# Kernel optimization log

Measured on AMD Instinct MI355X. Metric: run time of the kernel, lower is better.

## Reference

```python
import jax, jax.numpy as jnp
import numpy as np

B, T, D = 2, 2048, 1024
H = 16
HD = D // H  # 64


def _rope_tables(t_len, hd, dtype=jnp.float32):
    inv_freq = 1.0 / (10000.0 ** (jnp.arange(0, hd, 2, dtype=jnp.float32) / hd))
    freqs = jnp.outer(jnp.arange(t_len, dtype=jnp.float32), inv_freq)  # [T, hd/2]
    emb = jnp.concatenate([freqs, freqs], axis=-1)  # [T, hd]
    return emb.astype(dtype)


def _rotate_half(x):
    x1, x2 = jnp.split(x, 2, axis=-1)
    return jnp.concatenate([-x2, x1], axis=-1)


def setup_inputs() -> dict:
    key = jax.random.key(0)
    k1, k2, k3 = jax.random.split(key, 3)
    x = jax.random.normal(k1, (B, T, D), dtype=jnp.float32)
    w_qkv = jax.random.normal(k2, (D, 3 * D), dtype=jnp.float32) * (D ** -0.5)
    w_out = jax.random.normal(k3, (D, D), dtype=jnp.float32) * (D ** -0.5)
    return {"x": x, "w_qkv": w_qkv, "w_out": w_out}


def reference(x, w_qkv, w_out):
    Bc, Tc, Dc = x.shape
    scale = HD ** -0.5
    qkv = x @ w_qkv  # [B,T,3D]
    q, k, v = jnp.split(qkv, 3, axis=-1)
    # -> [B,H,T,hd]
    q = q.reshape(Bc, Tc, H, HD).transpose(0, 2, 1, 3)
    k = k.reshape(Bc, Tc, H, HD).transpose(0, 2, 1, 3)
    v = v.reshape(Bc, Tc, H, HD).transpose(0, 2, 1, 3)
    emb = _rope_tables(Tc, HD, x.dtype)  # [T,hd]
    cos = jnp.cos(emb)[None, None, :, :]
    sin = jnp.sin(emb)[None, None, :, :]
    q = q * cos + _rotate_half(q) * sin
    k = k * cos + _rotate_half(k) * sin
    attn = jnp.einsum('bhqd,bhkd->bhqk', q, k) * scale  # [B,H,T,T]
    causal = jnp.tril(jnp.ones((Tc, Tc), dtype=bool))
    attn = jnp.where(causal[None, None], attn, -jnp.inf)
    attn = jax.nn.softmax(attn, axis=-1)
    out = jnp.einsum('bhqk,bhkd->bhqd', attn, v)
    out = out.transpose(0, 2, 1, 3).reshape(Bc, Tc, Dc)
    return out @ w_out
```

## Files before the change

### kernel.cpp

```cpp
#include <hip/hip_runtime.h>

#define TSEQ 2048
#define DMODEL 1024
#define NHEAD 16
#define HDIM 64
#define NB 2
#define MROWS 4096
#define NQKV 3072
#define QSCALE 0.1803368801111204f
#define ROPE_C (13.2877123795494f / 32.0f)
#define NEGINF -3.0e38f

using s16x8 = __attribute__((ext_vector_type(8))) short;
using s16x4 = __attribute__((ext_vector_type(4))) short;
using f32x4 = __attribute__((ext_vector_type(4))) float;
using u32x2 = __attribute__((ext_vector_type(2))) unsigned int;

static __device__ __forceinline__ float b2f(unsigned short u) {
  union { unsigned int i; float f; } x; x.i = ((unsigned int)u) << 16; return x.f;
}
static __device__ __forceinline__ unsigned short f2b(float f) {
  unsigned int u = __float_as_uint(f);
  u += 0x7fffu + ((u >> 16) & 1u);
  return (unsigned short)(u >> 16);
}

#if __has_builtin(__builtin_amdgcn_exp2f)
#define EXP2(x) __builtin_amdgcn_exp2f(x)
#else
#define EXP2(x) exp2f(x)
#endif

typedef const __attribute__((address_space(1))) char gchar;
typedef __attribute__((address_space(3))) char lchar;
static __device__ __forceinline__ void gload_lds16(const void* g, void* l) {
  __builtin_amdgcn_global_load_lds((gchar*)g, (lchar*)l, 16, 0, 0);
}

__global__ __launch_bounds__(256) void k_prep(const float* __restrict__ x,
                                              short* __restrict__ xb,
                                              const float* __restrict__ wq,
                                              short* __restrict__ wqT,
                                              const float* __restrict__ wo,
                                              short* __restrict__ woT) {
  __shared__ float tile[32][33];
  const int blk = blockIdx.x;
  const int tid = threadIdx.x;
  if (blk < 4096) {
    const int i = blk * 256 + tid;
    const float4 v = ((const float4*)x)[i];
    s16x4 o;
    o.x = (short)f2b(v.x); o.y = (short)f2b(v.y);
    o.z = (short)f2b(v.z); o.w = (short)f2b(v.w);
    ((s16x4*)xb)[i] = o;
    return;
  }
  const float* in; short* out; int C, bx, by;
  if (blk < 7168) {
    const int l = blk - 4096; in = wq; out = wqT; C = NQKV;
    bx = l % 96; by = l / 96;
  } else {
    const int l = blk - 7168; in = wo; out = woT; C = DMODEL;
    bx = l & 31; by = l >> 5;
  }
  const int tx = tid & 31, ty4 = (tid >> 5) * 4;
#pragma unroll
  for (int i = 0; i < 4; ++i)
    tile[ty4 + i][tx] = in[(by * 32 + ty4 + i) * C + bx * 32 + tx];
  __syncthreads();
#pragma unroll
  for (int i = 0; i < 4; ++i)
    out[(bx * 32 + ty4 + i) * DMODEL + by * 32 + tx] = (short)f2b(tile[tx][ty4 + i]);
}

__global__ __launch_bounds__(256) void k_gemm_qkv(const short* __restrict__ A,
                                                  const short* __restrict__ BT,
                                                  short* __restrict__ Qo,
                                                  short* __restrict__ Ko,
                                                  short* __restrict__ Vt) {
  __shared__ __attribute__((aligned(16))) short As[128 * 64];
  __shared__ __attribute__((aligned(16))) short Bs[128 * 64];
  const int K = DMODEL;
  const int tid = threadIdx.x;
  const int wave = tid >> 6, lane = tid & 63, quad = lane >> 4, l15 = lane & 15;
  const int wm = (wave >> 1) * 64, wn = (wave & 1) * 64;
  const int bid = blockIdx.y * 24 + blockIdx.x;
  const int swz = (bid & 7) * 96 + (bid >> 3);
  const int bx = swz % 24, by = swz / 24;
  const int m0 = by * 128, n0 = bx * 128;
  f32x4 acc[4][4] = {};
  const char* Ab = (const char*)A;
  const char* Bb = (const char*)BT;
  char* AsB = (char*)As;
  char* BsB = (char*)Bs;
  int srow[4], scg[4], ssw[4];
#pragma unroll
  for (int p = 0; p < 4; ++p) {
    const int i = p * 256 + tid;
    srow[p] = i >> 3;
    scg[p] = i & 7;
    ssw[p] = scg[p] ^ (srow[p] & 7);
  }
#define QLOAD(k0v)                                                            \
  do {                                                                        \
    _Pragma("unroll")                                                         \
    for (int p = 0; p < 4; ++p) {                                             \
      ra[p] = *(const f32x4*)(Ab + ((long)(m0 + srow[p]) * K + (k0v)) * 2 + scg[p] * 16); \
      rb[p] = *(const f32x4*)(Bb + ((long)(n0 + srow[p]) * K + (k0v)) * 2 + scg[p] * 16); \
    }                                                                         \
  } while (0)
#define QWRITE()                                                              \
  do {                                                                        \
    _Pragma("unroll")                                                         \
    for (int p = 0; p < 4; ++p) {                                             \
      *(f32x4*)(AsB + srow[p] * 128 + ssw[p] * 16) = ra[p];                   \
      *(f32x4*)(BsB + srow[p] * 128 + ssw[p] * 16) = rb[p];                   \
    }                                                                         \
  } while (0)

  f32x4 ra[4], rb[4];
  const int nK = K / 64;
  QLOAD(0);
  QWRITE();
  __syncthreads();
  for (int kt = 0; kt < nK; ++kt) {
    if (kt + 1 < nK) QLOAD((kt + 1) * 64);
#pragma unroll
    for (int hf = 0; hf < 2; ++hf) {
      s16x8 af[4], bf[4];
#pragma unroll
      for (int i = 0; i < 4; ++i) {
        const int rowa = wm + i * 16 + l15;
        af[i] = *(const s16x8*)(AsB + rowa * 128 + (((hf * 4 + quad) ^ (rowa & 7)) * 16));
        const int rowb = wn + i * 16 + l15;
        bf[i] = *(const s16x8*)(BsB + rowb * 128 + (((hf * 4 + quad) ^ (rowb & 7)) * 16));
      }
#pragma unroll
      for (int i = 0; i < 4; ++i)
#pragma unroll
        for (int j = 0; j < 4; ++j)
          acc[i][j] = __builtin_amdgcn_mfma_f32_16x16x32_bf16(af[i], bf[j], acc[i][j], 0, 0, 0);
    }
    asm volatile("s_waitcnt lgkmcnt(0)" ::: "memory");
    __builtin_amdgcn_s_barrier();
    if (kt + 1 < nK) {
      QWRITE();
      asm volatile("s_waitcnt lgkmcnt(0)" ::: "memory");
      __builtin_amdgcn_s_barrier();
    }
  }
#undef QLOAD
#undef QWRITE
  const int colbase = n0 + wn;
  const int region = colbase >> 10;
  const int hh = (colbase & 1023) >> 6;
  const int bq = m0 >> 11;
  const int tbase = (m0 & 2047) + wm;
  char* sw = (wave < 2) ? (AsB + wave * 8192) : (BsB + (wave - 2) * 8192);
  if (region == 2) {
#pragma unroll
    for (int i = 0; i < 4; ++i)
#pragma unroll
      for (int j = 0; j < 4; ++j) {
        const int d = j * 16 + l15;
        const int t0 = i * 16 + quad * 4;
        s16x4 w;
        w.x = (short)f2b(acc[i][j][0]);
        w.y = (short)f2b(acc[i][j][1]);
        w.z = (short)f2b(acc[i][j][2]);
        w.w = (short)f2b(acc[i][j][3]);
        *(s16x4*)(sw + d * 128 + ((((t0 >> 3) ^ (d & 7))) * 16) + (t0 & 7) * 2) = w;
      }
    short* dstv = Vt + (((long)(bq * NHEAD + hh) * HDIM) << 11);
#pragma unroll
    for (int p = 0; p < 8; ++p) {
      const int linear = p * 64 + lane;
      const int d = linear >> 3, c = linear & 7;
      const s16x8 v = *(const s16x8*)(sw + d * 128 + ((c ^ (d & 7)) * 16));
      *(s16x8*)(dstv + (((long)d) << 11) + tbase + c * 8) = v;
    }
  } else {
    if (region == 1) {
#pragma unroll
      for (int i = 0; i < 4; ++i)
#pragma unroll
        for (int j = 0; j < 2; ++j) {
          const int d = j * 16 + l15;
          const float inv = exp2f(-(float)d * ROPE_C);
#pragma unroll
          for (int r = 0; r < 4; ++r) {
            const int t = tbase + i * 16 + quad * 4 + r;
            float sn, cs;
            __sincosf((float)t * inv, &sn, &cs);
            const float a = acc[i][j][r];
            const float bv = acc[i][j + 2][r];
            acc[i][j][r]     = a * cs - bv * sn;
            acc[i][j + 2][r] = bv * cs + a * sn;
          }
        }
    }
#pragma unroll
    for (int i = 0; i < 4; ++i)
#pragma unroll
      for (int j = 0; j < 4; ++j)
#pragma unroll
        for (int r = 0; r < 4; ++r) {
          const int row = i * 16 + quad * 4 + r;
          const int col = j * 16 + l15;
          *(short*)(sw + row * 128 + ((((col >> 3) ^ (row & 7))) * 16) + (col & 7) * 2)
              = (short)f2b(acc[i][j][r]);
        }
    short* dst = (region ? Ko : Qo) + ((long)(bq * NHEAD + hh) * TSEQ + tbase) * HDIM;
#pragma unroll
    for (int p = 0; p < 8; ++p) {
      const int linear = p * 64 + lane;
      const int r = linear >> 3, c = linear & 7;
      const s16x8 v = *(const s16x8*)(sw + r * 128 + ((c ^ (r & 7)) * 16));
      *(s16x8*)(dst + (long)r * HDIM + c * 8) = v;
    }
  }
}

template <int IM, bool OUT_BF16>
__global__ __launch_bounds__(256) void k_gemm(const short* __restrict__ A,
                                              const short* __restrict__ BT,
                                              void* __restrict__ Cv,
                                              int M, int N, int K) {
  static_assert(IM == 2, "vmcnt literal assumes IM==2 (6 loads/thread)");
  __shared__ __attribute__((aligned(16))) short As[2][IM * 32 * 64];
  __shared__ __attribute__((aligned(16))) short Bs[2][128 * 64];
  const int tid = threadIdx.x;
  const int wave = tid >> 6, lane = tid & 63, quad = lane >> 4, l15 = lane & 15;
  const int wm = (wave >> 1) * (IM * 16), wn = (wave & 1) * 64;
  const int nwg = gridDim.x * gridDim.y;
  const int bid = blockIdx.y * gridDim.x + blockIdx.x;
  const int swz = (bid & 7) * (nwg >> 3) + (bid >> 3);
  const int bx = swz % gridDim.x, by = swz / gridDim.x;
  const int m0 = by * (IM * 32), n0 = bx * 128;
  f32x4 acc[IM][4] = {};
  const char* Ab = (const char*)A;
  const char* Bb = (const char*)BT;
  char* AsB = (char*)As;
  char* BsB = (char*)Bs;
  int srow[4], sg[4];
#pragma unroll
  for (int p = 0; p < 4; ++p) {
    const int i = p * 256 + tid;
    srow[p] = i >> 3;
    sg[p] = (i & 7) ^ (srow[p] & 7);
  }
#define GSTAGE(k0v, buf)                                                       \
  do {                                                                         \
    _Pragma("unroll")                                                          \
    for (int p = 0; p < IM; ++p) {                                             \
      const long go = ((long)(m0 + srow[p]) * K + (k0v)) * 2 + sg[p] * 16;     \
      gload_lds16(Ab + go, AsB + (buf) * (IM * 4096) + p * 4096 + wave * 1024);\
    }                                                                          \
    _Pragma("unroll")                                                          \
    for (int p = 0; p < 4; ++p) {                                              \
      const long go = ((long)(n0 + srow[p]) * K + (k0v)) * 2 + sg[p] * 16;     \
      gload_lds16(Bb + go, BsB + (buf) * 16384 + p * 4096 + wave * 1024);      \
    }                                                                          \
  } while (0)

  const int nK = K / 64;
  GSTAGE(0, 0);
  for (int kt = 0; kt < nK; ++kt) {
    const int cur = kt & 1;
    if (kt + 1 < nK) {
      GSTAGE((kt + 1) * 64, cur ^ 1);
      asm volatile("s_waitcnt vmcnt(6)" ::: "memory");
    } else {
      asm volatile("s_waitcnt vmcnt(0)" ::: "memory");
    }
    __builtin_amdgcn_s_barrier();
    const char* Ac = AsB + cur * (IM * 4096);
    const char* Bc = BsB + cur * 16384;
#pragma unroll
    for (int hf = 0; hf < 2; ++hf) {
      s16x8 af[IM], bf[4];
#pragma unroll
      for (int i = 0; i < IM; ++i) {
        const int rowa = wm + i * 16 + l15;
        af[i] = *(const s16x8*)(Ac + rowa * 128 + (((hf * 4 + quad) ^ (rowa & 7)) * 16));
      }
#pragma unroll
      for (int j = 0; j < 4; ++j) {
        const int rowb = wn + j * 16 + l15;
        bf[j] = *(const s16x8*)(Bc + rowb * 128 + (((hf * 4 + quad) ^ (rowb & 7)) * 16));
      }
#pragma unroll
      for (int i = 0; i < IM; ++i)
#pragma unroll
        for (int j = 0; j < 4; ++j)
          acc[i][j] = __builtin_amdgcn_mfma_f32_16x16x32_bf16(af[i], bf[j], acc[i][j], 0, 0, 0);
    }
    asm volatile("s_waitcnt lgkmcnt(0)" ::: "memory");
    __builtin_amdgcn_s_barrier();
  }
#undef GSTAGE
  if (OUT_BF16) {
#pragma unroll
    for (int i = 0; i < IM; ++i) {
      const int row = m0 + wm + i * 16 + quad * 4;
#pragma unroll
      for (int j = 0; j < 4; ++j) {
        const int col = n0 + wn + j * 16 + l15;
#pragma unroll
        for (int r = 0; r < 4; ++r)
          ((short*)Cv)[(long)(row + r) * N + col] = (short)f2b(acc[i][j][r]);
      }
    }
  } else {
    char* sw = (char*)Bs + wave * 8192;
#pragma unroll
    for (int i = 0; i < IM; ++i)
#pragma unroll
      for (int j = 0; j < 4; ++j)
#pragma unroll
        for (int r = 0; r < 4; ++r) {
          const int row = i * 16 + quad * 4 + r;
          const int col = j * 16 + l15;
          *(float*)(sw + row * 256 + ((((col >> 2) ^ (row & 7))) * 16) + (col & 3) * 4)
              = acc[i][j][r];
        }
    float* C = (float*)Cv;
#pragma unroll
    for (int p = 0; p < 8; ++p) {
      const int linear = p * 64 + lane;
      const int r = linear >> 4, c = linear & 15;
      const f32x4 v = *(const f32x4*)(sw + r * 256 + ((c ^ (r & 7)) * 16));
      *(f32x4*)(C + (long)(m0 + wm + r) * N + n0 + wn + c * 4) = v;
    }
  }
}

__global__ __launch_bounds__(512) __attribute__((amdgpu_waves_per_eu(4)))
void k_attn(const short* __restrict__ Qg,
            const short* __restrict__ Kg,
            const short* __restrict__ Vg,
            short* __restrict__ O) {
  __shared__ __attribute__((aligned(16))) short Ks[2][64 * 64];
  __shared__ __attribute__((aligned(16))) short Vs[2][64 * 64];
  __shared__ __attribute__((aligned(16))) short pl[8][16 * 64];
  const int bx = blockIdx.x, by = blockIdx.y;
  const int qi = ((by >> 4) & 1) ? (15 - bx) : bx;
  const int bh = by;
  const int b = bh >> 4, h = bh & 15;
  const int tid = threadIdx.x, wave = tid >> 6, lane = tid & 63;
  const int quad = lane >> 4, l15 = lane & 15;
  const char* Kb = (const char*)(Kg + (long)bh * TSEQ * HDIM);
  const char* Vb = (const char*)(Vg + (long)bh * HDIM * TSEQ);
  const short* Qb = Qg + (long)bh * TSEQ * HDIM;
  const int qr0 = qi * 128 + wave * 16;
  const s16x8 rq0 = *(const s16x8*)&Qb[(qr0 + l15) * HDIM + quad * 8];
  const s16x8 rq1 = *(const s16x8*)&Qb[(qr0 + l15) * HDIM + 32 + quad * 8];
  s16x8 aq0, aq1;
  {
    const float tf = (float)(qr0 + l15);
#pragma unroll
    for (int j = 0; j < 8; ++j) {
      const float inv = exp2f(-(float)(quad * 8 + j) * ROPE_C);
      float sn, cs;
      __sincosf(tf * inv, &sn, &cs);
      sn *= QSCALE; cs *= QSCALE;
      const float q0 = b2f((unsigned short)rq0[j]);
      const float q1 = b2f((unsigned short)rq1[j]);
      aq0[j] = (short)f2b(q0 * cs - q1 * sn);
      aq1[j] = (short)f2b(q1 * cs + q0 * sn);
    }
  }
  s16x8 ones;
#pragma unroll
  for (int j = 0; j < 8; ++j) ones[j] = (short)0x3F80;
  f32x4 o[4] = {};
  f32x4 zs = {};
  const int kr0 = tid >> 3, kg0 = (tid & 7) ^ (kr0 & 7);
  char* KsB = (char*)Ks;
  char* VsB = (char*)Vs;
  char* plwB = (char*)pl + wave * 2048;
  const int ldsw = wave * 1024;

#define STAGE(kjv, buf)                                                     \
  do {                                                                      \
    gload_lds16(Kb + (kjv) * 8192 + (kr0 * 8 + kg0) * 16,                   \
                KsB + (buf) * 8192 + ldsw);                                 \
    gload_lds16(Vb + (kjv) * 128 + kr0 * (TSEQ * 2) + kg0 * 16,             \
                VsB + (buf) * 8192 + ldsw);                                 \
  } while (0)

  STAGE(0, 0);

  const int kjmax = 2 * qi + 1;
  const int kjd = qr0 >> 6;
  for (int kj = 0; kj <= kjmax; ++kj) {
    const int cur = kj & 1;
    if (kj < kjmax) {
      STAGE(kj + 1, cur ^ 1);
      asm volatile("s_waitcnt vmcnt(2)" ::: "memory");
    } else {
      asm volatile("s_waitcnt vmcnt(0)" ::: "memory");
    }
    __builtin_amdgcn_s_barrier();
    if (kj <= kjd) {
      const char* kb = KsB + cur * 8192;
      const char* vb = VsB + cur * 8192;
      f32x4 s[4];
      __builtin_amdgcn_s_setprio(1);
#pragma unroll
      for (int j2 = 0; j2 < 4; ++j2) {
        const int row = j2 * 16 + l15;
        const s16x8 k0 = *(const s16x8*)(kb + row * 128 + ((quad ^ (row & 7)) * 16));
        const s16x8 k1 = *(const s16x8*)(kb + row * 128 + (((4 + quad) ^ (row & 7)) * 16));
        f32x4 z = {};
        z = __builtin_amdgcn_mfma_f32_16x16x32_bf16(k0, aq0, z, 0, 0, 0);
        z = __builtin_amdgcn_mfma_f32_16x16x32_bf16(k1, aq1, z, 0, 0, 0);
        s[j2] = z;
      }
      __builtin_amdgcn_s_setprio(0);
      if (kj == kjd) {
        const int qloc = (qr0 & 63) + l15;
#pragma unroll
        for (int j2 = 0; j2 < 4; ++j2)
#pragma unroll
          for (int r = 0; r < 4; ++r)
            if (j2 * 16 + quad * 4 + r > qloc) s[j2][r] = NEGINF;
      }
#pragma unroll
      for (int j2 = 0; j2 < 4; ++j2) {
        const unsigned int u0 = __float_as_uint(EXP2(s[j2][0])) & 0xffff0000u;
        const unsigned int u1 = __float_as_uint(EXP2(s[j2][1])) & 0xffff0000u;
        const unsigned int u2 = __float_as_uint(EXP2(s[j2][2])) & 0xffff0000u;
        const unsigned int u3 = __float_as_uint(EXP2(s[j2][3])) & 0xffff0000u;
        u32x2 w;
        w.x = (u0 >> 16) | u1;
        w.y = (u2 >> 16) | u3;
        const int t0 = j2 * 16 + quad * 4;
        *(u32x2*)(plwB + l15 * 128 + (((t0 >> 3) ^ (l15 & 7)) * 16) + (quad & 1) * 8) = w;
      }
      const s16x8 bp0 = *(const s16x8*)(plwB + l15 * 128 + ((quad ^ (l15 & 7)) * 16));
      const s16x8 bp1 = *(const s16x8*)(plwB + l15 * 128 + (((4 + quad) ^ (l15 & 7)) * 16));
      __builtin_amdgcn_s_setprio(1);
      zs = __builtin_amdgcn_mfma_f32_16x16x32_bf16(ones, bp0, zs, 0, 0, 0);
      zs = __builtin_amdgcn_mfma_f32_16x16x32_bf16(ones, bp1, zs, 0, 0, 0);
#pragma unroll
      for (int hs = 0; hs < 4; ++hs) {
        const int d = hs * 16 + l15;
        const s16x8 av0 = *(const s16x8*)(vb + d * 128 + ((quad ^ (d & 7)) * 16));
        const s16x8 av1 = *(const s16x8*)(vb + d * 128 + (((4 + quad) ^ (d & 7)) * 16));
        o[hs] = __builtin_amdgcn_mfma_f32_16x16x32_bf16(av0, bp0, o[hs], 0, 0, 0);
        o[hs] = __builtin_amdgcn_mfma_f32_16x16x32_bf16(av1, bp1, o[hs], 0, 0, 0);
      }
      __builtin_amdgcn_s_setprio(0);
    }
    asm volatile("s_waitcnt lgkmcnt(0)" ::: "memory");
    __builtin_amdgcn_s_barrier();
  }
#undef STAGE
  const float rinv = 1.0f / zs[0];
  const int t = qr0 + l15;
  short* Orow = O + (long)(b * TSEQ + t) * DMODEL + h * HDIM + quad * 4;
#pragma unroll
  for (int hs = 0; hs < 4; ++hs) {
    s16x4 w;
    w.x = (short)f2b(o[hs][0] * rinv);
    w.y = (short)f2b(o[hs][1] * rinv);
    w.z = (short)f2b(o[hs][2] * rinv);
    w.w = (short)f2b(o[hs][3] * rinv);
    *(s16x4*)(Orow + hs * 16) = w;
  }
}

extern "C" void kernel_launch(void* const* d_in, const int* in_sizes, int n_in,
                              void* d_out, int out_size, void* d_ws, size_t ws_size,
                              hipStream_t stream) {
  const float* x = (const float*)d_in[0];
  const float* w_qkv = (const float*)d_in[1];
  const float* w_out = (const float*)d_in[2];
  float* out = (float*)d_out;
  char* ws = (char*)d_ws;

  short* xb    = (short*)(ws);
  short* wqkvT = (short*)(ws + (8ll << 20));
  short* woutT = (short*)(ws + (14ll << 20));
  short* Qb    = (short*)(ws + (16ll << 20));
  short* Kb    = (short*)(ws + (24ll << 20));
  short* Vt    = (short*)(ws + (32ll << 20));
  short* Ob    = (short*)(ws + (40ll << 20));

  k_prep<<<dim3(8192), dim3(256), 0, stream>>>(x, xb, w_qkv, wqkvT, w_out, woutT);
  k_gemm_qkv<<<dim3(NQKV / 128, MROWS / 128), dim3(256), 0, stream>>>(
      xb, wqkvT, Qb, Kb, Vt);
  k_attn<<<dim3(TSEQ / 128, NB * NHEAD), dim3(512), 0, stream>>>(Qb, Kb, Vt, Ob);
  k_gemm<2, false><<<dim3(DMODEL / 128, MROWS / 64), dim3(256), 0, stream>>>(
      Ob, woutT, (void*)out, MROWS, DMODEL, DMODEL);
}
```

Measured before the change: 176.2 us.

## Use 128x128 tiles with register-staged prefetch for output projection GEMM

Replaces the generic 64x128 output-projection GEMM with a dedicated 128x128 tile kernel in which each wave computes a 64x64 sub-tile. Direct global-to-LDS double buffering is replaced by a single LDS buffer, with the next K tile prefetched into registers and written after compute. This raises MFMA work per LDS fragment load and halves the grid to 256 blocks, at the cost of more registers, an extra barrier per iteration, and fewer blocks to fill the CUs.

```diff
diff --git a/kernel.cpp b/kernel.cpp
--- a/kernel.cpp
+++ b/kernel.cpp
@@ -221,116 +221,103 @@
   }
 }
 
-template <int IM, bool OUT_BF16>
-__global__ __launch_bounds__(256) void k_gemm(const short* __restrict__ A,
-                                              const short* __restrict__ BT,
-                                              void* __restrict__ Cv,
-                                              int M, int N, int K) {
-  static_assert(IM == 2, "vmcnt literal assumes IM==2 (6 loads/thread)");
-  __shared__ __attribute__((aligned(16))) short As[2][IM * 32 * 64];
-  __shared__ __attribute__((aligned(16))) short Bs[2][128 * 64];
+__global__ __launch_bounds__(256) void k_gemm_o(const short* __restrict__ A,
+                                                const short* __restrict__ BT,
+                                                float* __restrict__ C) {
+  __shared__ __attribute__((aligned(16))) short As[128 * 64];
+  __shared__ __attribute__((aligned(16))) short Bs[128 * 64];
+  const int K = DMODEL;
+  const int N = DMODEL;
   const int tid = threadIdx.x;
   const int wave = tid >> 6, lane = tid & 63, quad = lane >> 4, l15 = lane & 15;
-  const int wm = (wave >> 1) * (IM * 16), wn = (wave & 1) * 64;
-  const int nwg = gridDim.x * gridDim.y;
-  const int bid = blockIdx.y * gridDim.x + blockIdx.x;
-  const int swz = (bid & 7) * (nwg >> 3) + (bid >> 3);
-  const int bx = swz % gridDim.x, by = swz / gridDim.x;
-  const int m0 = by * (IM * 32), n0 = bx * 128;
-  f32x4 acc[IM][4] = {};
+  const int wm = (wave >> 1) * 64, wn = (wave & 1) * 64;
+  const int bid = blockIdx.y * 8 + blockIdx.x;
+  const int swz = (bid & 7) * 32 + (bid >> 3);
+  const int bx = swz & 7, by = swz >> 3;
+  const int m0 = by * 128, n0 = bx * 128;
+  f32x4 acc[4][4] = {};
   const char* Ab = (const char*)A;
   const char* Bb = (const char*)BT;
   char* AsB = (char*)As;
   char* BsB = (char*)Bs;
-  int srow[4], sg[4];
+  int srow[4], scg[4], ssw[4];
 #pragma unroll
   for (int p = 0; p < 4; ++p) {
     const int i = p * 256 + tid;
     srow[p] = i >> 3;
-    sg[p] = (i & 7) ^ (srow[p] & 7);
-  }
-#define GSTAGE(k0v, buf)                                                       \
-  do {                                                                         \
-    _Pragma("unroll")                                                          \
-    for (int p = 0; p < IM; ++p) {                                             \
-      const long go = ((long)(m0 + srow[p]) * K + (k0v)) * 2 + sg[p] * 16;     \
-      gload_lds16(Ab + go, AsB + (buf) * (IM * 4096) + p * 4096 + wave * 1024);\
-    }                                                                          \
-    _Pragma("unroll")                                                          \
-    for (int p = 0; p < 4; ++p) {                                              \
-      const long go = ((long)(n0 + srow[p]) * K + (k0v)) * 2 + sg[p] * 16;     \
-      gload_lds16(Bb + go, BsB + (buf) * 16384 + p * 4096 + wave * 1024);      \
-    }                                                                          \
+    scg[p] = i & 7;
+    ssw[p] = scg[p] ^ (srow[p] & 7);
+  }
+#define OLOAD(k0v)                                                            \
+  do {                                                                        \
+    _Pragma("unroll")                                                         \
+    for (int p = 0; p < 4; ++p) {                                             \
+      ra[p] = *(const f32x4*)(Ab + ((long)(m0 + srow[p]) * K + (k0v)) * 2 + scg[p] * 16); \
+      rb[p] = *(const f32x4*)(Bb + ((long)(n0 + srow[p]) * K + (k0v)) * 2 + scg[p] * 16); \
+    }                                                                         \
   } while (0)
-
+#define OWRITE()                                                              \
+  do {                                                                        \
+    _Pragma("unroll")                                                         \
+    for (int p = 0; p < 4; ++p) {                                             \
+      *(f32x4*)(AsB + srow[p] * 128 + ssw[p] * 16) = ra[p];                   \
+      *(f32x4*)(BsB + srow[p] * 128 + ssw[p] * 16) = rb[p];                   \
+    }                                                                         \
+  } while (0)
+
+  f32x4 ra[4], rb[4];
   const int nK = K / 64;
-  GSTAGE(0, 0);
+  OLOAD(0);
+  OWRITE();
+  __syncthreads();
   for (int kt = 0; kt < nK; ++kt) {
-    const int cur = kt & 1;
-    if (kt + 1 < nK) {
-      GSTAGE((kt + 1) * 64, cur ^ 1);
-      asm volatile("s_waitcnt vmcnt(6)" ::: "memory");
-    } else {
-      asm volatile("s_waitcnt vmcnt(0)" ::: "memory");
-    }
-    __builtin_amdgcn_s_barrier();
-    const char* Ac = AsB + cur * (IM * 4096);
-    const char* Bc = BsB + cur * 16384;
+    if (kt + 1 < nK) OLOAD((kt + 1) * 64);
 #pragma unroll
     for (int hf = 0; hf < 2; ++hf) {
-      s16x8 af[IM], bf[4];
-#pragma unroll
-      for (int i = 0; i < IM; ++i) {
+      s16x8 af[4], bf[4];
+#pragma unroll
+      for (int i = 0; i < 4; ++i) {
         const int rowa = wm + i * 16 + l15;
-        af[i] = *(const s16x8*)(Ac + rowa * 128 + (((hf * 4 + quad) ^ (rowa & 7)) * 16));
-      }
-#pragma unroll
-      for (int j = 0; j < 4; ++j) {
-        const int rowb = wn + j * 16 + l15;
-        bf[j] = *(const s16x8*)(Bc + rowb * 128 + (((hf * 4 + quad) ^ (rowb & 7)) * 16));
-      }
-#pragma unroll
-      for (int i = 0; i < IM; ++i)
+        af[i] = *(const s16x8*)(AsB + rowa * 128 + (((hf * 4 + quad) ^ (rowa & 7)) * 16));
+        const int rowb = wn + i * 16 + l15;
+        bf[i] = *(const s16x8*)(BsB + rowb * 128 + (((hf * 4 + quad) ^ (rowb & 7)) * 16));
+      }
+#pragma unroll
+      for (int i = 0; i < 4; ++i)
 #pragma unroll
         for (int j = 0; j < 4; ++j)
           acc[i][j] = __builtin_amdgcn_mfma_f32_16x16x32_bf16(af[i], bf[j], acc[i][j], 0, 0, 0);
     }
     asm volatile("s_waitcnt lgkmcnt(0)" ::: "memory");
     __builtin_amdgcn_s_barrier();
-  }
-#undef GSTAGE
-  if (OUT_BF16) {
-#pragma unroll
-    for (int i = 0; i < IM; ++i) {
-      const int row = m0 + wm + i * 16 + quad * 4;
-#pragma unroll
-      for (int j = 0; j < 4; ++j) {
-        const int col = n0 + wn + j * 16 + l15;
-#pragma unroll
-        for (int r = 0; r < 4; ++r)
-          ((short*)Cv)[(long)(row + r) * N + col] = (short)f2b(acc[i][j][r]);
-      }
-    }
-  } else {
-    char* sw = (char*)Bs + wave * 8192;
-#pragma unroll
-    for (int i = 0; i < IM; ++i)
+    if (kt + 1 < nK) {
+      OWRITE();
+      asm volatile("s_waitcnt lgkmcnt(0)" ::: "memory");
+      __builtin_amdgcn_s_barrier();
+    }
+  }
+#undef OLOAD
+#undef OWRITE
+  char* sw = (wave < 2) ? (AsB + wave * 8192) : (BsB + (wave - 2) * 8192);
+#pragma unroll
+  for (int ih = 0; ih < 2; ++ih) {
+#pragma unroll
+    for (int i2 = 0; i2 < 2; ++i2)
 #pragma unroll
       for (int j = 0; j < 4; ++j)
 #pragma unroll
         for (int r = 0; r < 4; ++r) {
-          const int row = i * 16 + quad * 4 + r;
+          const int row = i2 * 16 + quad * 4 + r;
           const int col = j * 16 + l15;
           *(float*)(sw + row * 256 + ((((col >> 2) ^ (row & 7))) * 16) + (col & 3) * 4)
-              = acc[i][j][r];
+              = acc[ih * 2 + i2][j][r];
         }
-    float* C = (float*)Cv;
 #pragma unroll
     for (int p = 0; p < 8; ++p) {
       const int linear = p * 64 + lane;
       const int r = linear >> 4, c = linear & 15;
       const f32x4 v = *(const f32x4*)(sw + r * 256 + ((c ^ (r & 7)) * 16));
-      *(f32x4*)(C + (long)(m0 + wm + r) * N + n0 + wn + c * 4) = v;
+      *(f32x4*)(C + (long)(m0 + wm + ih * 32 + r) * N + n0 + wn + c * 4) = v;
     }
   }
 }
@@ -492,6 +479,6 @@
   k_gemm_qkv<<<dim3(NQKV / 128, MROWS / 128), dim3(256), 0, stream>>>(
       xb, wqkvT, Qb, Kb, Vt);
   k_attn<<<dim3(TSEQ / 128, NB * NHEAD), dim3(512), 0, stream>>>(Qb, Kb, Vt, Ob);
-  k_gemm<2, false><<<dim3(DMODEL / 128, MROWS / 64), dim3(256), 0, stream>>>(
-      Ob, woutT, (void*)out, MROWS, DMODEL, DMODEL);
-}
+  k_gemm_o<<<dim3(DMODEL / 128, MROWS / 128), dim3(256), 0, stream>>>(
+      Ob, woutT, out);
+}
```

Result: slower. 183.9 us (+4.4%).

## Rewrite attention kernel with 32x32x16 MFMA tiles and register-shuffled probabilities

Applied to the files above, without the earlier changes.

The attention kernel now runs 4 waves of 32 query rows each and uses 32x32x16 bf16 MFMAs for both QK^T and PV. The probability matrix is passed between the two matmuls with cross-half lane shuffles instead of a per-wave LDS round trip. The row sum is computed in registers instead of with an extra ones-vector MFMA. Each thread now stages twice as many K/V chunks. The change targets LDS traffic and MFMA issue overhead, at the cost of fewer threads per block and higher register pressure.

```diff
diff --git a/kernel.cpp b/kernel.cpp
--- a/kernel.cpp
+++ b/kernel.cpp
@@ -14,7 +14,9 @@
 using s16x8 = __attribute__((ext_vector_type(8))) short;
 using s16x4 = __attribute__((ext_vector_type(4))) short;
 using f32x4 = __attribute__((ext_vector_type(4))) float;
+using f32x16 = __attribute__((ext_vector_type(16))) float;
 using u32x2 = __attribute__((ext_vector_type(2))) unsigned int;
+using u32x4 = __attribute__((ext_vector_type(4))) unsigned int;
 
 static __device__ __forceinline__ float b2f(unsigned short u) {
   union { unsigned int i; float f; } x; x.i = ((unsigned int)u) << 16; return x.f;
@@ -23,6 +25,11 @@
   unsigned int u = __float_as_uint(f);
   u += 0x7fffu + ((u >> 16) & 1u);
   return (unsigned short)(u >> 16);
+}
+static __device__ __forceinline__ unsigned rbf(float f) {
+  unsigned u = __float_as_uint(f);
+  u = (u + 0x7fffu + ((u >> 16) & 1u)) & 0xffff0000u;
+  return u;
 }
 
 #if __has_builtin(__builtin_amdgcn_exp2f)
@@ -335,69 +342,72 @@
   }
 }
 
-__global__ __launch_bounds__(512) __attribute__((amdgpu_waves_per_eu(4)))
-void k_attn(const short* __restrict__ Qg,
-            const short* __restrict__ Kg,
-            const short* __restrict__ Vg,
-            short* __restrict__ O) {
+__global__ __launch_bounds__(256, 2) void k_attn(const short* __restrict__ Qg,
+                                                 const short* __restrict__ Kg,
+                                                 const short* __restrict__ Vg,
+                                                 short* __restrict__ O) {
   __shared__ __attribute__((aligned(16))) short Ks[2][64 * 64];
   __shared__ __attribute__((aligned(16))) short Vs[2][64 * 64];
-  __shared__ __attribute__((aligned(16))) short pl[8][16 * 64];
   const int bx = blockIdx.x, by = blockIdx.y;
   const int qi = ((by >> 4) & 1) ? (15 - bx) : bx;
-  const int bh = by;
-  const int b = bh >> 4, h = bh & 15;
+  const int bh = by, b = bh >> 4, h = bh & 15;
   const int tid = threadIdx.x, wave = tid >> 6, lane = tid & 63;
-  const int quad = lane >> 4, l15 = lane & 15;
+  const int H = lane >> 5, q5 = lane & 31;
   const char* Kb = (const char*)(Kg + (long)bh * TSEQ * HDIM);
   const char* Vb = (const char*)(Vg + (long)bh * HDIM * TSEQ);
   const short* Qb = Qg + (long)bh * TSEQ * HDIM;
-  const int qr0 = qi * 128 + wave * 16;
-  const s16x8 rq0 = *(const s16x8*)&Qb[(qr0 + l15) * HDIM + quad * 8];
-  const s16x8 rq1 = *(const s16x8*)&Qb[(qr0 + l15) * HDIM + 32 + quad * 8];
-  s16x8 aq0, aq1;
+  const int qbase = qi * 128 + wave * 32;
+  const int kjmax = 2 * qi + 1;
+  const int kjd = qbase >> 6;
+
+  s16x8 qf[4];
+#pragma unroll
+  for (int dk = 0; dk < 4; ++dk)
+    qf[dk] = *(const s16x8*)&Qb[(qbase + q5) * HDIM + dk * 16 + H * 8];
   {
-    const float tf = (float)(qr0 + l15);
-#pragma unroll
-    for (int j = 0; j < 8; ++j) {
-      const float inv = exp2f(-(float)(quad * 8 + j) * ROPE_C);
-      float sn, cs;
-      __sincosf(tf * inv, &sn, &cs);
-      sn *= QSCALE; cs *= QSCALE;
-      const float q0 = b2f((unsigned short)rq0[j]);
-      const float q1 = b2f((unsigned short)rq1[j]);
-      aq0[j] = (short)f2b(q0 * cs - q1 * sn);
-      aq1[j] = (short)f2b(q1 * cs + q0 * sn);
-    }
-  }
-  s16x8 ones;
-#pragma unroll
-  for (int j = 0; j < 8; ++j) ones[j] = (short)0x3F80;
-  f32x4 o[4] = {};
-  f32x4 zs = {};
-  const int kr0 = tid >> 3, kg0 = (tid & 7) ^ (kr0 & 7);
+    const float tf = (float)(qbase + q5);
+#pragma unroll
+    for (int dk = 0; dk < 2; ++dk)
+#pragma unroll
+      for (int j = 0; j < 8; ++j) {
+        const int d = dk * 16 + H * 8 + j;
+        const float inv = exp2f(-(float)d * ROPE_C);
+        float sn, cs;
+        __sincosf(tf * inv, &sn, &cs);
+        sn *= QSCALE; cs *= QSCALE;
+        const float a0 = b2f((unsigned short)qf[dk][j]);
+        const float a1 = b2f((unsigned short)qf[dk + 2][j]);
+        qf[dk][j] = (short)f2b(a0 * cs - a1 * sn);
+        qf[dk + 2][j] = (short)f2b(a1 * cs + a0 * sn);
+      }
+  }
+  f32x16 o0 = {}, o1 = {};
+  float lsum = 0.0f;
+  const int r0 = tid >> 3,        g0 = (tid & 7) ^ (r0 & 7);
+  const int r1 = 32 + (tid >> 3), g1 = (tid & 7) ^ (r1 & 7);
   char* KsB = (char*)Ks;
   char* VsB = (char*)Vs;
-  char* plwB = (char*)pl + wave * 2048;
   const int ldsw = wave * 1024;
 
 #define STAGE(kjv, buf)                                                     \
   do {                                                                      \
-    gload_lds16(Kb + (kjv) * 8192 + (kr0 * 8 + kg0) * 16,                   \
+    gload_lds16(Kb + (kjv) * 8192 + (r0 * 8 + g0) * 16,                     \
                 KsB + (buf) * 8192 + ldsw);                                 \
-    gload_lds16(Vb + (kjv) * 128 + kr0 * (TSEQ * 2) + kg0 * 16,             \
+    gload_lds16(Kb + (kjv) * 8192 + (r1 * 8 + g1) * 16,                     \
+                KsB + (buf) * 8192 + 4096 + ldsw);                          \
+    gload_lds16(Vb + (kjv) * 128 + r0 * (TSEQ * 2) + g0 * 16,               \
                 VsB + (buf) * 8192 + ldsw);                                 \
+    gload_lds16(Vb + (kjv) * 128 + r1 * (TSEQ * 2) + g1 * 16,               \
+                VsB + (buf) * 8192 + 4096 + ldsw);                          \
   } while (0)
 
   STAGE(0, 0);
 
-  const int kjmax = 2 * qi + 1;
-  const int kjd = qr0 >> 6;
   for (int kj = 0; kj <= kjmax; ++kj) {
     const int cur = kj & 1;
     if (kj < kjmax) {
       STAGE(kj + 1, cur ^ 1);
-      asm volatile("s_waitcnt vmcnt(2)" ::: "memory");
+      asm volatile("s_waitcnt vmcnt(4)" ::: "memory");
     } else {
       asm volatile("s_waitcnt vmcnt(0)" ::: "memory");
     }
@@ -405,69 +415,96 @@
     if (kj <= kjd) {
       const char* kb = KsB + cur * 8192;
       const char* vb = VsB + cur * 8192;
-      f32x4 s[4];
+      f32x16 s0 = {}, s1 = {};
       __builtin_amdgcn_s_setprio(1);
 #pragma unroll
-      for (int j2 = 0; j2 < 4; ++j2) {
-        const int row = j2 * 16 + l15;
-        const s16x8 k0 = *(const s16x8*)(kb + row * 128 + ((quad ^ (row & 7)) * 16));
-        const s16x8 k1 = *(const s16x8*)(kb + row * 128 + (((4 + quad) ^ (row & 7)) * 16));
-        f32x4 z = {};
-        z = __builtin_amdgcn_mfma_f32_16x16x32_bf16(k0, aq0, z, 0, 0, 0);
-        z = __builtin_amdgcn_mfma_f32_16x16x32_bf16(k1, aq1, z, 0, 0, 0);
-        s[j2] = z;
+      for (int dk = 0; dk < 4; ++dk) {
+        const int c = dk * 2 + H;
+        const int ta = q5;
+        const s16x8 k0 = *(const s16x8*)(kb + ta * 128 + ((c ^ (ta & 7)) * 16));
+        s0 = __builtin_amdgcn_mfma_f32_32x32x16_bf16(k0, qf[dk], s0, 0, 0, 0);
+        const int tb = 32 + q5;
+        const s16x8 k1 = *(const s16x8*)(kb + tb * 128 + ((c ^ (tb & 7)) * 16));
+        s1 = __builtin_amdgcn_mfma_f32_32x32x16_bf16(k1, qf[dk], s1, 0, 0, 0);
       }
       __builtin_amdgcn_s_setprio(0);
       if (kj == kjd) {
-        const int qloc = (qr0 & 63) + l15;
-#pragma unroll
-        for (int j2 = 0; j2 < 4; ++j2)
-#pragma unroll
-          for (int r = 0; r < 4; ++r)
-            if (j2 * 16 + quad * 4 + r > qloc) s[j2][r] = NEGINF;
-      }
-#pragma unroll
-      for (int j2 = 0; j2 < 4; ++j2) {
-        const unsigned int u0 = __float_as_uint(EXP2(s[j2][0])) & 0xffff0000u;
-        const unsigned int u1 = __float_as_uint(EXP2(s[j2][1])) & 0xffff0000u;
-        const unsigned int u2 = __float_as_uint(EXP2(s[j2][2])) & 0xffff0000u;
-        const unsigned int u3 = __float_as_uint(EXP2(s[j2][3])) & 0xffff0000u;
-        u32x2 w;
-        w.x = (u0 >> 16) | u1;
-        w.y = (u2 >> 16) | u3;
-        const int t0 = j2 * 16 + quad * 4;
-        *(u32x2*)(plwB + l15 * 128 + (((t0 >> 3) ^ (l15 & 7)) * 16) + (quad & 1) * 8) = w;
-      }
-      const s16x8 bp0 = *(const s16x8*)(plwB + l15 * 128 + ((quad ^ (l15 & 7)) * 16));
-      const s16x8 bp1 = *(const s16x8*)(plwB + l15 * 128 + (((4 + quad) ^ (l15 & 7)) * 16));
-      __builtin_amdgcn_s_setprio(1);
-      zs = __builtin_amdgcn_mfma_f32_16x16x32_bf16(ones, bp0, zs, 0, 0, 0);
-      zs = __builtin_amdgcn_mfma_f32_16x16x32_bf16(ones, bp1, zs, 0, 0, 0);
-#pragma unroll
-      for (int hs = 0; hs < 4; ++hs) {
-        const int d = hs * 16 + l15;
-        const s16x8 av0 = *(const s16x8*)(vb + d * 128 + ((quad ^ (d & 7)) * 16));
-        const s16x8 av1 = *(const s16x8*)(vb + d * 128 + (((4 + quad) ^ (d & 7)) * 16));
-        o[hs] = __builtin_amdgcn_mfma_f32_16x16x32_bf16(av0, bp0, o[hs], 0, 0, 0);
-        o[hs] = __builtin_amdgcn_mfma_f32_16x16x32_bf16(av1, bp1, o[hs], 0, 0, 0);
-      }
-      __builtin_amdgcn_s_setprio(0);
+        const int qloc = (qbase & 63) + q5;
+#pragma unroll
+        for (int r = 0; r < 16; ++r) {
+          const int tl = (r & 3) + 8 * (r >> 2) + 4 * H;
+          if (tl > qloc) s0[r] = NEGINF;
+          if (tl + 32 > qloc) s1[r] = NEGINF;
+        }
+      }
+      unsigned pk[16];
+      float ps = 0.0f;
+#define PEXP(SV, TS)                                                        \
+      {                                                                     \
+        _Pragma("unroll")                                                   \
+        for (int g = 0; g < 4; ++g) {                                       \
+          const unsigned u0 = rbf(EXP2(SV[4 * g + 0]));                     \
+          const unsigned u1 = rbf(EXP2(SV[4 * g + 1]));                     \
+          const unsigned u2 = rbf(EXP2(SV[4 * g + 2]));                     \
+          const unsigned u3 = rbf(EXP2(SV[4 * g + 3]));                     \
+          ps += __uint_as_float(u0) + __uint_as_float(u1) +                 \
+                __uint_as_float(u2) + __uint_as_float(u3);                  \
+          pk[(TS) * 8 + g * 2]     = (u0 >> 16) | u1;                       \
+          pk[(TS) * 8 + g * 2 + 1] = (u2 >> 16) | u3;                       \
+        }                                                                   \
+      }
+      PEXP(s0, 0)
+      PEXP(s1, 1)
+#undef PEXP
+      lsum += ps;
+#pragma unroll
+      for (int ks = 0; ks < 4; ++ks) {
+        const int t8 = (ks >> 1) * 8;
+        const int a = (ks & 1) * 2;
+        const unsigned gA0 = pk[t8 + 2 * a + 0], gA1 = pk[t8 + 2 * a + 1];
+        const unsigned gB0 = pk[t8 + 2 * (a + 1) + 0], gB1 = pk[t8 + 2 * (a + 1) + 1];
+        const unsigned keep0 = H ? gB0 : gA0, keep1 = H ? gB1 : gA1;
+        const unsigned send0 = H ? gA0 : gB0, send1 = H ? gA1 : gB1;
+        const unsigned recv0 = __shfl_xor(send0, 32);
+        const unsigned recv1 = __shfl_xor(send1, 32);
+        union { u32x4 u; s16x8 s; } bp;
+        bp.u.x = H ? recv0 : keep0;
+        bp.u.y = H ? recv1 : keep1;
+        bp.u.z = H ? keep0 : recv0;
+        bp.u.w = H ? keep1 : recv1;
+        const int c = ks * 2 + H;
+        const int da = q5;
+        const s16x8 v0 = *(const s16x8*)(vb + da * 128 + ((c ^ (da & 7)) * 16));
+        const int db = 32 + q5;
+        const s16x8 v1 = *(const s16x8*)(vb + db * 128 + ((c ^ (db & 7)) * 16));
+        __builtin_amdgcn_s_setprio(1);
+        o0 = __builtin_amdgcn_mfma_f32_32x32x16_bf16(v0, bp.s, o0, 0, 0, 0);
+        o1 = __builtin_amdgcn_mfma_f32_32x32x16_bf16(v1, bp.s, o1, 0, 0, 0);
+        __builtin_amdgcn_s_setprio(0);
+      }
     }
     asm volatile("s_waitcnt lgkmcnt(0)" ::: "memory");
     __builtin_amdgcn_s_barrier();
   }
 #undef STAGE
-  const float rinv = 1.0f / zs[0];
-  const int t = qr0 + l15;
-  short* Orow = O + (long)(b * TSEQ + t) * DMODEL + h * HDIM + quad * 4;
-#pragma unroll
-  for (int hs = 0; hs < 4; ++hs) {
-    s16x4 w;
-    w.x = (short)f2b(o[hs][0] * rinv);
-    w.y = (short)f2b(o[hs][1] * rinv);
-    w.z = (short)f2b(o[hs][2] * rinv);
-    w.w = (short)f2b(o[hs][3] * rinv);
-    *(s16x4*)(Orow + hs * 16) = w;
+  lsum += __shfl_xor(lsum, 32);
+  const float rinv = 1.0f / lsum;
+  const int t = qbase + q5;
+  short* Orow = O + (long)(b * TSEQ + t) * DMODEL + h * HDIM;
+#pragma unroll
+  for (int rr = 0; rr < 4; ++rr) {
+    const int d0 = 8 * rr + 4 * H;
+    s16x4 w0, w1;
+    w0.x = (short)f2b(o0[4 * rr + 0] * rinv);
+    w0.y = (short)f2b(o0[4 * rr + 1] * rinv);
+    w0.z = (short)f2b(o0[4 * rr + 2] * rinv);
+    w0.w = (short)f2b(o0[4 * rr + 3] * rinv);
+    *(s16x4*)(Orow + d0) = w0;
+    w1.x = (short)f2b(o1[4 * rr + 0] * rinv);
+    w1.y = (short)f2b(o1[4 * rr + 1] * rinv);
+    w1.z = (short)f2b(o1[4 * rr + 2] * rinv);
+    w1.w = (short)f2b(o1[4 * rr + 3] * rinv);
+    *(s16x4*)(Orow + 32 + d0) = w1;
   }
 }
 
@@ -491,7 +528,7 @@
   k_prep<<<dim3(8192), dim3(256), 0, stream>>>(x, xb, w_qkv, wqkvT, w_out, woutT);
   k_gemm_qkv<<<dim3(NQKV / 128, MROWS / 128), dim3(256), 0, stream>>>(
       xb, wqkvT, Qb, Kb, Vt);
-  k_attn<<<dim3(TSEQ / 128, NB * NHEAD), dim3(512), 0, stream>>>(Qb, Kb, Vt, Ob);
+  k_attn<<<dim3(TSEQ / 128, NB * NHEAD), dim3(256), 0, stream>>>(Qb, Kb, Vt, Ob);
   k_gemm<2, false><<<dim3(DMODEL / 128, MROWS / 64), dim3(256), 0, stream>>>(
       Ob, woutT, (void*)out, MROWS, DMODEL, DMODEL);
 }
```

Measured after the change: 187.0 us. 1.06x slower.
